# Performance work log

Measured on AMD Instinct MI355X. Metric: run time of the kernel, lower is better.

Reference implementation:

```python
import jax, jax.numpy as jnp
import numpy as np

B, S, D = 2, 2048, 1024
NH, NKV = 16, 4
HD = D // NH          # 64
NREP = NH // NKV      # 4
E, TOPK = 8, 2
CAP_FACTOR = 1.25
HID = 4 * D // 3      # 1365 (hardcoded in MoELayer)
EPS = 1e-6


def rmsnorm(x, w):
    xf = x.astype(jnp.float32)
    y = xf * jax.lax.rsqrt(jnp.mean(xf * xf, axis=-1, keepdims=True) + EPS)
    return y.astype(x.dtype) * w


def apply_rope(x, cos, sin):
    # x: [b, s, h, hd]; cos/sin: [1, s, 1, hd]
    half = x.shape[-1] // 2
    x1, x2 = x[..., :half], x[..., half:]
    ch, sh = cos[..., :half], sin[..., :half]
    return jnp.concatenate([x1 * ch - x2 * sh, x1 * sh + x2 * ch], axis=-1)


def swiglu(x, w1, w2, w3):
    return (jax.nn.silu(x @ w1) * (x @ w3)) @ w2


def setup_inputs():
    key = jax.random.key(0)
    ks = jax.random.split(key, 14)
    x = jax.random.normal(ks[0], (B, S, D), jnp.float32)
    # RoPE tables (standard 10000 base), duplicated halves so cos[..., :half] is valid
    pos = jnp.arange(S, dtype=jnp.float32)[:, None]
    inv = 1.0 / (10000.0 ** (jnp.arange(0, HD, 2, dtype=jnp.float32) / HD))  # [HD/2]
    ang = pos * inv[None, :]                                                # [S, HD/2]
    cos = jnp.concatenate([jnp.cos(ang), jnp.cos(ang)], -1)[None, :, None, :]
    sin = jnp.concatenate([jnp.sin(ang), jnp.sin(ang)], -1)[None, :, None, :]
    # causal additive mask [1,1,S,S]
    causal = jnp.tril(jnp.ones((S, S), bool))
    mask = jnp.where(causal, 0.0, -1e9).astype(jnp.float32)[None, None]
    s = 0.02
    return {
        'x': x, 'cos': cos, 'sin': sin, 'mask': mask,
        'attn_norm_w': jnp.ones((D,), jnp.float32),
        'moe_norm_w': jnp.ones((D,), jnp.float32),
        'wq': jax.random.normal(ks[1], (D, NH * HD), jnp.float32) * s,
        'wk': jax.random.normal(ks[2], (D, NKV * HD), jnp.float32) * s,
        'wv': jax.random.normal(ks[3], (D, NKV * HD), jnp.float32) * s,
        'wo': jax.random.normal(ks[4], (NH * HD, D), jnp.float32) * s,
        'router_w': jax.random.normal(ks[5], (D, E), jnp.float32) * s,
        'ew1': jax.random.normal(ks[6], (E, D, HID), jnp.float32) * s,
        'ew2': jax.random.normal(ks[7], (E, HID, D), jnp.float32) * s,
        'ew3': jax.random.normal(ks[8], (E, D, HID), jnp.float32) * s,
        'sw1': jax.random.normal(ks[9], (D, HID), jnp.float32) * s,
        'sw2': jax.random.normal(ks[10], (HID, D), jnp.float32) * s,
        'sw3': jax.random.normal(ks[11], (D, HID), jnp.float32) * s,
    }


def reference(x, cos, sin, mask, attn_norm_w, moe_norm_w, wq, wk, wv, wo,
              router_w, ew1, ew2, ew3, sw1, sw2, sw3):
    # ---- attention path ----
    xn = rmsnorm(x, attn_norm_w)
    q = (xn @ wq).reshape(B, S, NH, HD)
    k = (xn @ wk).reshape(B, S, NKV, HD)
    v = (xn @ wv).reshape(B, S, NKV, HD)
    q = apply_rope(q, cos, sin)
    k = apply_rope(k, cos, sin)
    new_k, new_v = k, v  # kv cache outputs (no prior cache)
    # repeat_interleave kv heads to NH
    k_rep = jnp.repeat(k, NREP, axis=2)  # [b,s,NH,hd]
    v_rep = jnp.repeat(v, NREP, axis=2)
    scores = jnp.einsum('bqhd,bkhd->bhqk', q, k_rep) / np.sqrt(HD)
    scores = scores + mask[:, :, -S:, :]
    attn = jax.nn.softmax(scores.astype(jnp.float32), axis=-1).astype(q.dtype)
    ao = jnp.einsum('bhqk,bkhd->bqhd', attn, v_rep).reshape(B, S, NH * HD)
    h = x + ao @ wo

    # ---- MoE path ----
    hn = rmsnorm(h, moe_norm_w)
    x_flat = hn.reshape(-1, D)            # [T, D]
    T = x_flat.shape[0]
    logits = x_flat @ router_w            # [T, E]
    probs = jax.nn.softmax(logits, axis=-1)
    w_topk, idx = jax.lax.top_k(probs, TOPK)          # [T, K]
    w_topk = w_topk / jnp.sum(w_topk, axis=-1, keepdims=True)
    onehot = jax.nn.one_hot(idx, E, dtype=jnp.float32)  # [T, K, E]
    counts = jnp.sum(onehot, axis=(0, 1))               # [E]
    util = jnp.mean((counts > 0).astype(jnp.float32)) * 100.0
    fraction = counts / T
    aux_loss = E * jnp.sum(jnp.mean(probs, axis=0) * fraction)
    capacity = int(T * TOPK / E * CAP_FACTOR)
    member = jnp.sum(onehot, axis=1) > 0                 # [T, E] token assigned to expert
    keep = member & (jnp.cumsum(member.astype(jnp.int32), axis=0) <= capacity)
    gate = jnp.sum(w_topk[:, :, None] * onehot, axis=1)  # [T, E] combine weights
    gate = gate * keep.astype(gate.dtype)
    # dense per-expert SwiGLU (same math as masked dispatch; zero-gated tokens vanish)
    h1 = jnp.einsum('td,edh->eth', x_flat, ew1)
    h3 = jnp.einsum('td,edh->eth', x_flat, ew3)
    eo = jnp.einsum('eth,ehd->etd', jax.nn.silu(h1) * h3, ew2)
    moe_out = jnp.einsum('etd,te->td', eo, gate).reshape(B, S, D)
    moe_out = moe_out + swiglu(hn, sw1, sw2, sw3)  # shared expert

    out = h + moe_out
    return out, aux_loss, util, new_k, new_v
```

## Files before the change

kernel.cpp:

```cpp
#include <hip/hip_runtime.h>
#include <hip/hip_bf16.h>
#include <math.h>

typedef __hip_bfloat16 bf16;
typedef __attribute__((ext_vector_type(8))) short short8;
typedef __attribute__((ext_vector_type(4))) float floatx4;

#define SEQ    2048
#define TTOK   4096
#define DM     1024
#define NHEAD  16
#define NKVH   4
#define HD     64
#define NEXP   8
#define HIDDEN 1365
#define HIDP   1408
#define CAPT   1280
#define NSLOT  (NEXP*CAPT)
#define TSLOT  (NSLOT+TTOK)
#define XPE    (CAPT/128)
#define XBT    14

__device__ __forceinline__ void gld16(const void* g, void* l) {
  __builtin_amdgcn_global_load_lds((const __attribute__((address_space(1))) void*)g,
                                   (__attribute__((address_space(3))) void*)l,
                                   16, 0, 0);
}

struct __align__(8) bf4 { bf16 x, y, z, w; };

struct EpiAux {
  const float* cosb; const float* sinb;
  bf16* qb; bf16* kb; bf16* vb; float* newk; float* newv;
};

__global__ __launch_bounds__(256) void transpose_cvt(
    const float* __restrict__ src, bf16* __restrict__ dst,
    int K, int N, int Kp, long srcZ, long dstZ) {
  src += (size_t)blockIdx.z * srcZ;
  dst += (size_t)blockIdx.z * dstZ;
  __shared__ float tile[64][65];
  const int tid = threadIdx.x;
  const int k0 = blockIdx.y * 64, n0 = blockIdx.x * 64;
  const int lr = tid >> 4, lc = (tid & 15) * 4;
#pragma unroll
  for (int i = 0; i < 4; ++i) {
    int k = k0 + lr + i * 16;
    int n = n0 + lc;
    float4 v = {0.f, 0.f, 0.f, 0.f};
    if (k < K) {
      if (n + 3 < N) v = *(const float4*)(src + (size_t)k * N + n);
      else {
        float* vp = (float*)&v;
        for (int e = 0; e < 4; ++e) if (n + e < N) vp[e] = src[(size_t)k * N + n + e];
      }
    }
    tile[lr + i * 16][lc] = v.x; tile[lr + i * 16][lc + 1] = v.y;
    tile[lr + i * 16][lc + 2] = v.z; tile[lr + i * 16][lc + 3] = v.w;
  }
  __syncthreads();
  const int n = tid >> 2, kk0 = (tid & 3) * 16;
  if (n0 + n < N) {
    bf16 buf[16];
#pragma unroll
    for (int e = 0; e < 16; ++e) buf[e] = (bf16)tile[kk0 + e][n];
    bf16* dp = dst + (size_t)(n0 + n) * Kp + k0 + kk0;
    *(short8*)dp = *(short8*)buf;
    *(short8*)(dp + 8) = *(short8*)(buf + 8);
  }
}

__global__ __launch_bounds__(256) void rmsnorm_kernel(
    const float* __restrict__ x, const float* __restrict__ w, bf16* __restrict__ out) {
  int t = blockIdx.x;
  const float* xr = x + (size_t)t * DM;
  float4 xv = *(const float4*)(xr + threadIdx.x * 4);
  float ss = xv.x * xv.x + xv.y * xv.y + xv.z * xv.z + xv.w * xv.w;
#pragma unroll
  for (int off = 1; off < 64; off <<= 1) ss += __shfl_xor(ss, off);
  __shared__ float sred[4];
  if ((threadIdx.x & 63) == 0) sred[threadIdx.x >> 6] = ss;
  __syncthreads();
  float scale = rsqrtf((sred[0] + sred[1] + sred[2] + sred[3]) * (1.f / DM) + 1e-6f);
  float4 wv = *(const float4*)(w + threadIdx.x * 4);
  bf4 o;
  o.x = (bf16)(xv.x * scale * wv.x); o.y = (bf16)(xv.y * scale * wv.y);
  o.z = (bf16)(xv.z * scale * wv.z); o.w = (bf16)(xv.w * scale * wv.w);
  ((bf4*)(out + (size_t)t * DM))[threadIdx.x] = o;
}

__global__ __launch_bounds__(256) void rmsnorm_router_kernel(
    const float* __restrict__ x, const float* __restrict__ w, const float* __restrict__ rw,
    bf16* __restrict__ out, float* __restrict__ probs,
    int* __restrict__ tIdx, float* __restrict__ tW) {
  int t = blockIdx.x;
  int tid = threadIdx.x, lane = tid & 63, wv = tid >> 6;
  const float* xr = x + (size_t)t * DM;
  float4 xv = *(const float4*)(xr + tid * 4);
  float ss = xv.x * xv.x + xv.y * xv.y + xv.z * xv.z + xv.w * xv.w;
#pragma unroll
  for (int off = 1; off < 64; off <<= 1) ss += __shfl_xor(ss, off);
  __shared__ float sred[4];
  __shared__ float red[4][8];
  if (lane == 0) sred[wv] = ss;
  __syncthreads();
  float scale = rsqrtf((sred[0] + sred[1] + sred[2] + sred[3]) * (1.f / DM) + 1e-6f);
  float4 wvv = *(const float4*)(w + tid * 4);
  float y[4] = {xv.x * scale * wvv.x, xv.y * scale * wvv.y,
                xv.z * scale * wvv.z, xv.w * scale * wvv.w};
  bf4 o; o.x = (bf16)y[0]; o.y = (bf16)y[1]; o.z = (bf16)y[2]; o.w = (bf16)y[3];
  ((bf4*)(out + (size_t)t * DM))[tid] = o;
  float acc[8] = {0, 0, 0, 0, 0, 0, 0, 0};
#pragma unroll
  for (int dd = 0; dd < 4; ++dd) {
    const float* rwr = rw + (size_t)(tid * 4 + dd) * 8;
#pragma unroll
    for (int e = 0; e < 8; ++e) acc[e] += y[dd] * rwr[e];
  }
#pragma unroll
  for (int e = 0; e < 8; ++e)
#pragma unroll
    for (int off = 1; off < 64; off <<= 1) acc[e] += __shfl_xor(acc[e], off);
  if (lane == 0)
#pragma unroll
    for (int e = 0; e < 8; ++e) red[wv][e] = acc[e];
  __syncthreads();
  if (tid == 0) {
    float lg[8];
#pragma unroll
    for (int e = 0; e < 8; ++e) lg[e] = red[0][e] + red[1][e] + red[2][e] + red[3][e];
    float mx = lg[0];
#pragma unroll
    for (int e = 1; e < 8; ++e) mx = fmaxf(mx, lg[e]);
    float p[8], se = 0.f;
#pragma unroll
    for (int e = 0; e < 8; ++e) { p[e] = __expf(lg[e] - mx); se += p[e]; }
#pragma unroll
    for (int e = 0; e < 8; ++e) { p[e] /= se; probs[t * 8 + e] = p[e]; }
    int i1 = 0;
#pragma unroll
    for (int e = 1; e < 8; ++e) if (p[e] > p[i1]) i1 = e;
    int i2 = (i1 == 0) ? 1 : 0;
#pragma unroll
    for (int e = 0; e < 8; ++e) if (e != i1 && p[e] > p[i2]) i2 = e;
    float s = p[i1] + p[i2];
    tIdx[t * 2] = i1; tIdx[t * 2 + 1] = i2;
    tW[t * 2] = p[i1] / s; tW[t * 2 + 1] = p[i2] / s;
  }
}

template <int EPI>
__global__ __launch_bounds__(256) void gemm_bt(
    const bf16* __restrict__ A, const bf16* __restrict__ Bt,
    int M, int N, int K, int lda, int ldb, int xPerXcd,
    float* __restrict__ Cf, int ldc,
    const float* __restrict__ resid, EpiAux aux) {
  __shared__ __align__(16) bf16 As[128 * 64];
  __shared__ __align__(16) bf16 Bs[128 * 64];
  const int tid = threadIdx.x, lane = tid & 63, wave = tid >> 6;
  const int f = blockIdx.x, lo = f >> 3;
  int xb = (f & 7) * xPerXcd + lo % xPerXcd;
  int n0 = (lo / xPerXcd) * 128;
  int m0 = xb * 128;

  const bf16* aSrc[4]; const bf16* bSrc[4];
  bf16* aDst[4]; bf16* bDst[4];
#pragma unroll
  for (int it = 0; it < 4; ++it) {
    int c = it * 256 + tid;
    int r = c >> 3, q = c & 7;
    int kq = q ^ (r & 7);
    aSrc[it] = A + (long)(m0 + r) * lda + kq * 8;
    bSrc[it] = Bt + (long)(n0 + r) * ldb + kq * 8;
    aDst[it] = As + (size_t)(it * 256 + wave * 64) * 8;
    bDst[it] = Bs + (size_t)(it * 256 + wave * 64) * 8;
  }

  floatx4 acc[4][4];
#pragma unroll
  for (int i = 0; i < 4; ++i)
#pragma unroll
    for (int j = 0; j < 4; ++j) { floatx4 z = {0.f, 0.f, 0.f, 0.f}; acc[i][j] = z; }

  const int wm = (wave & 1) * 64, wn = (wave >> 1) * 64;
  const int l15 = lane & 15, quad = lane >> 4;
  int aOff[4][2], bOff[4][2];
#pragma unroll
  for (int i = 0; i < 4; ++i) {
    int m = wm + i * 16 + l15;
    int n = wn + i * 16 + l15;
#pragma unroll
    for (int h = 0; h < 2; ++h) {
      aOff[i][h] = (((m << 3) | ((h * 4 + quad) ^ (m & 7))) << 3);
      bOff[i][h] = (((n << 3) | ((h * 4 + quad) ^ (n & 7))) << 3);
    }
  }

  const int kIters = K >> 6;
  for (int kt = 0; kt < kIters; ++kt) {
    __syncthreads();
#pragma unroll
    for (int it = 0; it < 4; ++it) {
      gld16(aSrc[it], aDst[it]);
      gld16(bSrc[it], bDst[it]);
      aSrc[it] += 64; bSrc[it] += 64;
    }
    __syncthreads();
#pragma unroll
    for (int h = 0; h < 2; ++h) {
      short8 af[4], bfr[4];
#pragma unroll
      for (int i = 0; i < 4; ++i) af[i] = *(const short8*)(As + aOff[i][h]);
#pragma unroll
      for (int j = 0; j < 4; ++j) bfr[j] = *(const short8*)(Bs + bOff[j][h]);
#pragma unroll
      for (int i = 0; i < 4; ++i)
#pragma unroll
        for (int j = 0; j < 4; ++j)
          acc[i][j] = __builtin_amdgcn_mfma_f32_16x16x32_bf16(af[i], bfr[j], acc[i][j], 0, 0, 0);
    }
  }

  if constexpr (EPI == 4) {
#pragma unroll
    for (int i = 0; i < 4; ++i) {
#pragma unroll
      for (int r = 0; r < 4; ++r) {
        int row = wm + i * 16 + quad * 4 + r;
        int t = m0 + row;
        int s = t & (SEQ - 1);
        if (n0 < 1024) {
#pragma unroll
          for (int j = 0; j < 2; ++j) {
            int col = n0 + wn + j * 16 + l15;
            int dlo = col & 63;
            float x1 = acc[i][j][r], x2 = acc[i][j + 2][r];
            float ch = aux.cosb[s * 64 + dlo], sh = aux.sinb[s * 64 + dlo];
            aux.qb[(size_t)t * DM + col]      = (bf16)((x1 * ch - x2 * sh) * 0.125f);
            aux.qb[(size_t)t * DM + col + 32] = (bf16)((x1 * sh + x2 * ch) * 0.125f);
          }
        } else if (n0 < 1280) {
#pragma unroll
          for (int j = 0; j < 2; ++j) {
            int ck = n0 + wn + j * 16 + l15 - 1024;
            int dlo = ck & 63;
            float x1 = acc[i][j][r], x2 = acc[i][j + 2][r];
            float ch = aux.cosb[s * 64 + dlo], sh = aux.sinb[s * 64 + dlo];
            float o1 = x1 * ch - x2 * sh, o2 = x1 * sh + x2 * ch;
            aux.kb[(size_t)t * 256 + ck]        = (bf16)o1;
            aux.kb[(size_t)t * 256 + ck + 32]   = (bf16)o2;
            aux.newk[(size_t)t * 256 + ck]      = o1;
            aux.newk[(size_t)t * 256 + ck + 32] = o2;
          }
        } else {
#pragma unroll
          for (int j = 0; j < 4; ++j) {
            int cv = n0 + wn + j * 16 + l15 - 1280;
            float v = acc[i][j][r];
            aux.vb[(size_t)t * 256 + cv]   = (bf16)v;
            aux.newv[(size_t)t * 256 + cv] = v;
          }
        }
      }
    }
    return;
  }
#pragma unroll
  for (int i = 0; i < 4; ++i) {
#pragma unroll
    for (int j = 0; j < 4; ++j) {
      int col = n0 + wn + j * 16 + l15;
#pragma unroll
      for (int r = 0; r < 4; ++r) {
        int row = wm + i * 16 + quad * 4 + r;
        size_t o = (size_t)(m0 + row) * ldc + col;
        Cf[o] = resid[o] + acc[i][j][r];
      }
    }
  }
}

__device__ __forceinline__ bool slot_block(
    int f, int NY, const int* neCnt, int& expert, int& m0, int& mLimit, int& n0) {
  int xcd = f & 7, lo = f >> 3;
  int xb = lo / NY, y = lo % NY;
  n0 = y * 64;
  if (xb < XPE) {
    expert = xcd;
    int ne = neCnt[xcd];
    if (xb * 128 >= ne) return false;
    m0 = xcd * CAPT + xb * 128;
    mLimit = ne - xb * 128;
    if (mLimit > 128) mLimit = 128;
  } else {
    expert = 8;
    int sb = xcd * 4 + (xb - XPE);
    m0 = NSLOT + sb * 128;
    mLimit = 128;
  }
  return true;
}

__global__ __launch_bounds__(256) void gemm_dual9(
    const bf16* __restrict__ A, const bf16* __restrict__ B1t, const bf16* __restrict__ B3t,
    bf16* __restrict__ mact,
    const int* __restrict__ tokList, const int* __restrict__ neCnt) {
  __shared__ __align__(16) bf16 As[128 * 64];
  __shared__ __align__(16) bf16 B1s[64 * 64];
  __shared__ __align__(16) bf16 B3s[64 * 64];
  const int tid = threadIdx.x, lane = tid & 63, wave = tid >> 6;
  int expert, m0, mLimit, n0;
  if (!slot_block(blockIdx.x, 22, neCnt, expert, m0, mLimit, n0)) return;
  const bf16* B1e = B1t + (long)expert * (HIDDEN * 1024);
  const bf16* B3e = B3t + (long)expert * (HIDDEN * 1024);

  const bf16* aSrc[4]; const bf16* b1Src[2]; const bf16* b3Src[2];
  bf16* aDst[4]; bf16* b1Dst[2]; bf16* b3Dst[2];
#pragma unroll
  for (int it = 0; it < 4; ++it) {
    int c = it * 256 + tid;
    int r = c >> 3, q = c & 7;
    int kq = q ^ (r & 7);
    int rr = r < mLimit ? r : (mLimit - 1);
    aSrc[it] = A + (long)tokList[m0 + rr] * 1024 + kq * 8;
    aDst[it] = As + (size_t)(it * 256 + wave * 64) * 8;
  }
#pragma unroll
  for (int it = 0; it < 2; ++it) {
    int c = it * 256 + tid;
    int r = c >> 3, q = c & 7;
    int kq = q ^ (r & 7);
    int nn = n0 + r; if (nn > HIDDEN - 1) nn = HIDDEN - 1;
    b1Src[it] = B1e + (long)nn * 1024 + kq * 8;
    b3Src[it] = B3e + (long)nn * 1024 + kq * 8;
    b1Dst[it] = B1s + (size_t)(it * 256 + wave * 64) * 8;
    b3Dst[it] = B3s + (size_t)(it * 256 + wave * 64) * 8;
  }

  floatx4 acc1[4][2], acc3[4][2];
#pragma unroll
  for (int i = 0; i < 4; ++i)
#pragma unroll
    for (int j = 0; j < 2; ++j) {
      floatx4 z = {0.f, 0.f, 0.f, 0.f};
      acc1[i][j] = z; acc3[i][j] = z;
    }

  const int wm = (wave & 1) * 64, wn = (wave >> 1) * 32;
  const int l15 = lane & 15, quad = lane >> 4;
  int aOff[4][2], bOff[2][2];
#pragma unroll
  for (int h = 0; h < 2; ++h) {
#pragma unroll
    for (int i = 0; i < 4; ++i) {
      int m = wm + i * 16 + l15;
      aOff[i][h] = (((m << 3) | ((h * 4 + quad) ^ (m & 7))) << 3);
    }
#pragma unroll
    for (int j = 0; j < 2; ++j) {
      int n = wn + j * 16 + l15;
      bOff[j][h] = (((n << 3) | ((h * 4 + quad) ^ (n & 7))) << 3);
    }
  }

  for (int kt = 0; kt < 16; ++kt) {
    __syncthreads();
#pragma unroll
    for (int it = 0; it < 4; ++it) { gld16(aSrc[it], aDst[it]); aSrc[it] += 64; }
#pragma unroll
    for (int it = 0; it < 2; ++it) {
      gld16(b1Src[it], b1Dst[it]); b1Src[it] += 64;
      gld16(b3Src[it], b3Dst[it]); b3Src[it] += 64;
    }
    __syncthreads();
#pragma unroll
    for (int h = 0; h < 2; ++h) {
      short8 af[4];
#pragma unroll
      for (int i = 0; i < 4; ++i) af[i] = *(const short8*)(As + aOff[i][h]);
#pragma unroll
      for (int j = 0; j < 2; ++j) {
        short8 b1f = *(const short8*)(B1s + bOff[j][h]);
        short8 b3f = *(const short8*)(B3s + bOff[j][h]);
#pragma unroll
        for (int i = 0; i < 4; ++i) {
          acc1[i][j] = __builtin_amdgcn_mfma_f32_16x16x32_bf16(af[i], b1f, acc1[i][j], 0, 0, 0);
          acc3[i][j] = __builtin_amdgcn_mfma_f32_16x16x32_bf16(af[i], b3f, acc3[i][j], 0, 0, 0);
        }
      }
    }
  }

#pragma unroll
  for (int i = 0; i < 4; ++i) {
#pragma unroll
    for (int j = 0; j < 2; ++j) {
      int col = n0 + wn + j * 16 + l15;
#pragma unroll
      for (int r = 0; r < 4; ++r) {
        int row = wm + i * 16 + quad * 4 + r;
        if (row >= mLimit) continue;
        float a1 = acc1[i][j][r], a3 = acc3[i][j][r];
        float sl = a1 / (1.f + __expf(-a1));
        mact[(size_t)(m0 + row) * HIDP + col] = (col < HIDDEN) ? (bf16)(sl * a3) : (bf16)0.f;
      }
    }
  }
}

__global__ __launch_bounds__(256) void gemm_down9(
    const bf16* __restrict__ A, const bf16* __restrict__ B2t,
    bf16* __restrict__ eo,
    const float* __restrict__ gateW, const int* __restrict__ neCnt) {
  __shared__ __align__(16) bf16 As[128 * 64];
  __shared__ __align__(16) bf16 Bs[64 * 64];
  const int tid = threadIdx.x, lane = tid & 63, wave = tid >> 6;
  int expert, m0, mLimit, n0;
  if (!slot_block(blockIdx.x, 16, neCnt, expert, m0, mLimit, n0)) return;
  const bf16* Be = B2t + (long)expert * (1024 * HIDP);

  const bf16* aSrc[4]; const bf16* bSrc[2];
  bf16* aDst[4]; bf16* bDst[2];
#pragma unroll
  for (int it = 0; it < 4; ++it) {
    int c = it * 256 + tid;
    int r = c >> 3, q = c & 7;
    int kq = q ^ (r & 7);
    int rr = r < mLimit ? r : (mLimit - 1);
    aSrc[it] = A + (long)(m0 + rr) * HIDP + kq * 8;
    aDst[it] = As + (size_t)(it * 256 + wave * 64) * 8;
  }
#pragma unroll
  for (int it = 0; it < 2; ++it) {
    int c = it * 256 + tid;
    int r = c >> 3, q = c & 7;
    int kq = q ^ (r & 7);
    bSrc[it] = Be + (long)(n0 + r) * HIDP + kq * 8;
    bDst[it] = Bs + (size_t)(it * 256 + wave * 64) * 8;
  }

  floatx4 acc[4][2];
#pragma unroll
  for (int i = 0; i < 4; ++i)
#pragma unroll
    for (int j = 0; j < 2; ++j) { floatx4 z = {0.f, 0.f, 0.f, 0.f}; acc[i][j] = z; }

  const int wm = (wave & 1) * 64, wn = (wave >> 1) * 32;
  const int l15 = lane & 15, quad = lane >> 4;
  int aOff[4][2], bOff[2][2];
#pragma unroll
  for (int h = 0; h < 2; ++h) {
#pragma unroll
    for (int i = 0; i < 4; ++i) {
      int m = wm + i * 16 + l15;
      aOff[i][h] = (((m << 3) | ((h * 4 + quad) ^ (m & 7))) << 3);
    }
#pragma unroll
    for (int j = 0; j < 2; ++j) {
      int n = wn + j * 16 + l15;
      bOff[j][h] = (((n << 3) | ((h * 4 + quad) ^ (n & 7))) << 3);
    }
  }

  for (int kt = 0; kt < 22; ++kt) {
    __syncthreads();
#pragma unroll
    for (int it = 0; it < 4; ++it) { gld16(aSrc[it], aDst[it]); aSrc[it] += 64; }
#pragma unroll
    for (int it = 0; it < 2; ++it) { gld16(bSrc[it], bDst[it]); bSrc[it] += 64; }
    __syncthreads();
#pragma unroll
    for (int h = 0; h < 2; ++h) {
      short8 af[4];
#pragma unroll
      for (int i = 0; i < 4; ++i) af[i] = *(const short8*)(As + aOff[i][h]);
#pragma unroll
      for (int j = 0; j < 2; ++j) {
        short8 bf = *(const short8*)(Bs + bOff[j][h]);
#pragma unroll
        for (int i = 0; i < 4; ++i)
          acc[i][j] = __builtin_amdgcn_mfma_f32_16x16x32_bf16(af[i], bf, acc[i][j], 0, 0, 0);
      }
    }
  }

#pragma unroll
  for (int i = 0; i < 4; ++i) {
#pragma unroll
    for (int j = 0; j < 2; ++j) {
      int col = n0 + wn + j * 16 + l15;
#pragma unroll
      for (int r = 0; r < 4; ++r) {
        int row = wm + i * 16 + quad * 4 + r;
        if (row >= mLimit) continue;
        eo[(size_t)(m0 + row) * 1024 + col] = (bf16)(gateW[m0 + row] * acc[i][j][r]);
      }
    }
  }
}

__global__ __launch_bounds__(256) void vt_kernel(
    const bf16* __restrict__ vb, bf16* __restrict__ vt) {
  __shared__ __align__(16) bf16 tile[64 * 72];
  int t0 = blockIdx.x * 64, bg = blockIdx.y;
  int b = bg >> 2, g = bg & 3;
  int tid = threadIdx.x;
  for (int c = tid; c < 512; c += 256) {
    int r = c >> 3, d8 = (c & 7) * 8;
    *(short8*)(tile + r * 72 + d8) =
        *(const short8*)(vb + (size_t)(b * SEQ + t0 + r) * 256 + g * 64 + d8);
  }
  __syncthreads();
  for (int c = tid; c < 512; c += 256) {
    int d = c >> 3, s8 = (c & 7) * 8;
    bf16 tmp[8];
#pragma unroll
    for (int x = 0; x < 8; ++x) tmp[x] = tile[(s8 + x) * 72 + d];
    *(short8*)(vt + ((size_t)bg * 64 + d) * SEQ + t0 + s8) = *(short8*)tmp;
  }
}

__global__ __launch_bounds__(256) void attn_kernel(
    const bf16* __restrict__ Q, const bf16* __restrict__ Kc, const bf16* __restrict__ Vt,
    bf16* __restrict__ AO) {
  __shared__ __align__(16) bf16 Qs[64 * 64];
  __shared__ __align__(16) bf16 Ks[64 * 64];
  __shared__ __align__(16) bf16 Vs[64 * 64];
  __shared__ __align__(16) bf16 Ps[4][16 * 64];
  const int pairI = blockIdx.x, h = blockIdx.y, b = blockIdx.z;
  const int g = h >> 2;
  const int tid = threadIdx.x, lane = tid & 63, wave = tid >> 6;
  const int l15 = lane & 15, quad = lane >> 4;

  const bf16* kSrc[2]; const bf16* vSrc[2]; bf16* kDst[2]; bf16* vDst[2];
#pragma unroll
  for (int it = 0; it < 2; ++it) {
    int c = it * 256 + tid;
    int r = c >> 3, p = c & 7;
    int kq = p ^ (r & 7);
    kSrc[it] = Kc + (size_t)(b * SEQ + r) * 256 + g * 64 + kq * 8;
    vSrc[it] = Vt + ((size_t)(b * 4 + g) * 64 + r) * SEQ + kq * 8;
    kDst[it] = Ks + (size_t)(it * 256 + wave * 64) * 8;
    vDst[it] = Vs + (size_t)(it * 256 + wave * 64) * 8;
  }

  int qOff[2], kvOff[4][2], pOff[2];
#pragma unroll
  for (int hh = 0; hh < 2; ++hh) {
    int m = wave * 16 + l15;
    qOff[hh] = (m << 6) + (((hh * 4 + quad) ^ (m & 7)) << 3);
#pragma unroll
    for (int j = 0; j < 4; ++j) {
      int n = j * 16 + l15;
      kvOff[j][hh] = (n << 6) + (((hh * 4 + quad) ^ (n & 7)) << 3);
    }
    int cblk = (hh * 2 + (quad >> 1)) ^ (l15 >> 2);
    pOff[hh] = (l15 << 6) + (cblk << 4) + ((quad & 1) << 3);
  }
  bf16* pw = &Ps[wave][0];
  const int rowl = wave * 16 + quad * 4;

  short8 onesb;
#pragma unroll
  for (int e = 0; e < 8; ++e) onesb[e] = (short)0x3F80;

  for (int ph = 0; ph < 2; ++ph) {
    const int q0 = (ph == 0 ? pairI : 31 - pairI) * 64;
    __syncthreads();
#pragma unroll
    for (int it = 0; it < 2; ++it) {
      int c = it * 256 + tid;
      int r = c >> 3, p = c & 7;
      int kq = p ^ (r & 7);
      gld16(Q + (size_t)(b * SEQ + q0 + r) * DM + h * 64 + kq * 8,
            Qs + (size_t)(it * 256 + wave * 64) * 8);
    }

    floatx4 oacc[4], sumacc;
#pragma unroll
    for (int r = 0; r < 4; ++r) { floatx4 z = {0.f, 0.f, 0.f, 0.f}; oacc[r] = z; }
    { floatx4 z = {0.f, 0.f, 0.f, 0.f}; sumacc = z; }

    const int nkt = (q0 >> 6) + 1;
    for (int kt = 0; kt < nkt; ++kt) {
      __syncthreads();
#pragma unroll
      for (int it = 0; it < 2; ++it) {
        gld16(kSrc[it] + (size_t)kt * 64 * 256, kDst[it]);
        gld16(vSrc[it] + kt * 64, vDst[it]);
      }
      __syncthreads();

      floatx4 sacc[4];
#pragma unroll
      for (int j = 0; j < 4; ++j) { floatx4 z = {0.f, 0.f, 0.f, 0.f}; sacc[j] = z; }
#pragma unroll
      for (int hh = 0; hh < 2; ++hh) {
        short8 aq = *(const short8*)(Qs + qOff[hh]);
#pragma unroll
        for (int j = 0; j < 4; ++j)
          sacc[j] = __builtin_amdgcn_mfma_f32_16x16x32_bf16(
              aq, *(const short8*)(Ks + kvOff[j][hh]), sacc[j], 0, 0, 0);
      }

      const bool lastTile = (kt == nkt - 1);
#pragma unroll
      for (int j = 0; j < 4; ++j) {
        int sw = ((j ^ quad) << 4) + l15;
        int colg = j * 16 + l15;
#pragma unroll
        for (int r = 0; r < 4; ++r) {
          float p = __expf(sacc[j][r]);
          if (lastTile && colg > rowl + r) p = 0.f;
          pw[(quad * 4 + r) * 64 + sw] = (bf16)p;
        }
      }
      asm volatile("s_waitcnt lgkmcnt(0)" ::: "memory");
#pragma unroll
      for (int hh = 0; hh < 2; ++hh) {
        short8 ap = *(const short8*)(pw + pOff[hh]);
#pragma unroll
        for (int j = 0; j < 4; ++j)
          oacc[j] = __builtin_amdgcn_mfma_f32_16x16x32_bf16(
              ap, *(const short8*)(Vs + kvOff[j][hh]), oacc[j], 0, 0, 0);
        sumacc = __builtin_amdgcn_mfma_f32_16x16x32_bf16(ap, onesb, sumacc, 0, 0, 0);
      }
    }

    float inv[4];
#pragma unroll
    for (int r = 0; r < 4; ++r) inv[r] = 1.f / sumacc[r];
#pragma unroll
    for (int j = 0; j < 4; ++j)
#pragma unroll
      for (int r = 0; r < 4; ++r) {
        int t = b * SEQ + q0 + rowl + r;
        AO[(size_t)t * DM + h * 64 + j * 16 + l15] = (bf16)(oacc[j][r] * inv[r]);
      }
  }
}

__global__ __launch_bounds__(256) void assign_kernel(
    const int* __restrict__ tIdx, const float* __restrict__ tW,
    int* __restrict__ tokList, float* __restrict__ gateW,
    int* __restrict__ neCnt, int* __restrict__ cntFull, int* __restrict__ slotOf) {
  int e = blockIdx.x;
  int tid = threadIdx.x, lane = tid & 63, wv = tid >> 6;
  if (e == 8) {
    for (int t = tid; t < TTOK; t += 256) {
      tokList[NSLOT + t] = t;
      gateW[NSLOT + t] = 1.0f;
    }
    if (tid == 0) neCnt[8] = TTOK;
    return;
  }
  __shared__ int waveTot[4];
  __shared__ int offs;
  if (tid == 0) offs = 0;
  __syncthreads();
  for (int base = 0; base < TTOK; base += 256) {
    int t = base + tid;
    int a = tIdx[t * 2], b2 = tIdx[t * 2 + 1];
    bool sel = (a == e) || (b2 == e);
    unsigned long long mask = __ballot(sel);
    int wrank = __popcll(mask & ((1ull << lane) - 1ull));
    if (lane == 0) waveTot[wv] = __popcll(mask);
    __syncthreads();
    int pre = offs;
    for (int w2 = 0; w2 < wv; ++w2) pre += waveTot[w2];
    int rank = pre + wrank;
    if (sel && rank < CAPT) {
      int slot = e * CAPT + rank;
      tokList[slot] = t;
      gateW[slot] = (a == e) ? tW[t * 2] : tW[t * 2 + 1];
      slotOf[t * 2 + ((a == e) ? 0 : 1)] = slot;
    }
    __syncthreads();
    if (tid == 0) offs += waveTot[0] + waveTot[1] + waveTot[2] + waveTot[3];
    __syncthreads();
  }
  if (tid == 0) {
    cntFull[e] = offs;
    neCnt[e] = offs < CAPT ? offs : CAPT;
  }
}

__global__ __launch_bounds__(256) void aux_kernel(
    const float* __restrict__ probs, const int* __restrict__ cntFull,
    float* __restrict__ outAux) {
  __shared__ float psum[8];
  if (threadIdx.x < 8) psum[threadIdx.x] = 0.f;
  __syncthreads();
  float lp[8] = {0, 0, 0, 0, 0, 0, 0, 0};
  for (int t = threadIdx.x; t < TTOK; t += 256) {
#pragma unroll
    for (int e = 0; e < 8; ++e) lp[e] += probs[t * 8 + e];
  }
#pragma unroll
  for (int e = 0; e < 8; ++e)
#pragma unroll
    for (int off = 1; off < 64; off <<= 1) lp[e] += __shfl_xor(lp[e], off);
  if ((threadIdx.x & 63) == 0)
#pragma unroll
    for (int e = 0; e < 8; ++e) atomicAdd(&psum[e], lp[e]);
  __syncthreads();
  if (threadIdx.x == 0) {
    float aux = 0.f; int used = 0;
    for (int e = 0; e < 8; ++e) {
      aux += (psum[e] / (float)TTOK) * ((float)cntFull[e] / (float)TTOK);
      if (cntFull[e] > 0) used++;
    }
    outAux[0] = 8.f * aux;
    outAux[1] = 100.f * (float)used / 8.f;
  }
}

__global__ __launch_bounds__(256) void combine_kernel(
    float* __restrict__ outp, const float* __restrict__ hbuf,
    const bf16* __restrict__ eo, const int* __restrict__ slotOf) {
  int t = blockIdx.x, tid = threadIdx.x;
  float4 v = ((const float4*)(hbuf + (size_t)t * DM))[tid];
  bf4 sh = ((const bf4*)(eo + (size_t)(NSLOT + t) * DM))[tid];
  v.x += (float)sh.x; v.y += (float)sh.y; v.z += (float)sh.z; v.w += (float)sh.w;
  int s0 = slotOf[t * 2], s1 = slotOf[t * 2 + 1];
  if (s0 >= 0) {
    bf4 e = ((const bf4*)(eo + (size_t)s0 * DM))[tid];
    v.x += (float)e.x; v.y += (float)e.y; v.z += (float)e.z; v.w += (float)e.w;
  }
  if (s1 >= 0) {
    bf4 e = ((const bf4*)(eo + (size_t)s1 * DM))[tid];
    v.x += (float)e.x; v.y += (float)e.y; v.z += (float)e.z; v.w += (float)e.w;
  }
  ((float4*)(outp + (size_t)t * DM))[tid] = v;
}

extern "C" void kernel_launch(void* const* d_in, const int* in_sizes, int n_in,
                              void* d_out, int out_size, void* d_ws, size_t ws_size,
                              hipStream_t stream) {
  (void)in_sizes; (void)n_in; (void)out_size; (void)ws_size;
  const float* x     = (const float*)d_in[0];
  const float* cosb  = (const float*)d_in[1];
  const float* sinb  = (const float*)d_in[2];
  const float* attnw = (const float*)d_in[4];
  const float* moew  = (const float*)d_in[5];
  const float* wq  = (const float*)d_in[6];
  const float* wk  = (const float*)d_in[7];
  const float* wv  = (const float*)d_in[8];
  const float* wo  = (const float*)d_in[9];
  const float* rw  = (const float*)d_in[10];
  const float* ew1 = (const float*)d_in[11];
  const float* ew2 = (const float*)d_in[12];
  const float* ew3 = (const float*)d_in[13];
  const float* sw1 = (const float*)d_in[14];
  const float* sw2 = (const float*)d_in[15];
  const float* sw3 = (const float*)d_in[16];

  float* outp = (float*)d_out;
  float* auxp = outp + 4194304;
  float* newk = outp + 4194306;
  float* newv = newk + 1048576;

  char* wsp = (char*)d_ws;
  size_t off = 0;
  auto alloc = [&](size_t bytes) -> void* {
    void* p = wsp + off; off += (bytes + 255) & ~(size_t)255; return p;
  };
  bf16* wqkvT = (bf16*)alloc((size_t)1536 * 1024 * 2);
  bf16* woT   = (bf16*)alloc((size_t)1024 * 1024 * 2);
  bf16* ew1T  = (bf16*)alloc((size_t)9 * HIDDEN * 1024 * 2);
  bf16* ew3T  = (bf16*)alloc((size_t)9 * HIDDEN * 1024 * 2);
  bf16* ew2T  = (bf16*)alloc((size_t)9 * 1024 * HIDP * 2);
  bf16* xn    = (bf16*)alloc((size_t)TTOK * DM * 2);
  bf16* qb    = (bf16*)alloc((size_t)TTOK * DM * 2);
  bf16* kb    = (bf16*)alloc((size_t)TTOK * 256 * 2);
  bf16* vb    = (bf16*)alloc((size_t)TTOK * 256 * 2);
  bf16* vt    = (bf16*)alloc((size_t)TTOK * 256 * 2);
  bf16* ao    = (bf16*)alloc((size_t)TTOK * DM * 2);
  float* hbuf = (float*)alloc((size_t)TTOK * DM * 4);
  bf16* hn    = (bf16*)alloc((size_t)TTOK * DM * 2);
  float* probs = (float*)alloc((size_t)TTOK * 8 * 4);
  int*   tIdx  = (int*)alloc((size_t)TTOK * 2 * 4);
  float* tW    = (float*)alloc((size_t)TTOK * 2 * 4);
  int*   tokList = (int*)alloc((size_t)TSLOT * 4);
  float* gateW   = (float*)alloc((size_t)TSLOT * 4);
  int*   neCnt   = (int*)alloc(64);
  int*   cntFull = (int*)alloc(64);
  int*   slotOf  = (int*)alloc((size_t)TTOK * 2 * 4);
  bf16*  mact = (bf16*)alloc((size_t)TSLOT * HIDP * 2);
  bf16*  eo   = (bf16*)alloc((size_t)TSLOT * DM * 2);

  EpiAux nil{};
  EpiAux ropeAux{cosb, sinb, qb, kb, vb, newk, newv};

  transpose_cvt<<<dim3(16, 16, 1), 256, 0, stream>>>(wq, wqkvT, 1024, 1024, 1024, 0, 0);
  transpose_cvt<<<dim3(4, 16, 1), 256, 0, stream>>>(wk, wqkvT + (size_t)1024 * 1024, 1024, 256, 1024, 0, 0);
  transpose_cvt<<<dim3(4, 16, 1), 256, 0, stream>>>(wv, wqkvT + (size_t)1280 * 1024, 1024, 256, 1024, 0, 0);
  transpose_cvt<<<dim3(16, 16, 1), 256, 0, stream>>>(wo, woT, 1024, 1024, 1024, 0, 0);
  transpose_cvt<<<dim3(22, 16, NEXP), 256, 0, stream>>>(ew1, ew1T, 1024, HIDDEN, 1024,
      (long)1024 * HIDDEN, (long)HIDDEN * 1024);
  transpose_cvt<<<dim3(22, 16, NEXP), 256, 0, stream>>>(ew3, ew3T, 1024, HIDDEN, 1024,
      (long)1024 * HIDDEN, (long)HIDDEN * 1024);
  transpose_cvt<<<dim3(16, 22, NEXP), 256, 0, stream>>>(ew2, ew2T, HIDDEN, 1024, HIDP,
      (long)HIDDEN * 1024, (long)1024 * HIDP);
  transpose_cvt<<<dim3(22, 16, 1), 256, 0, stream>>>(sw1, ew1T + (size_t)8 * HIDDEN * 1024,
      1024, HIDDEN, 1024, 0, 0);
  transpose_cvt<<<dim3(22, 16, 1), 256, 0, stream>>>(sw3, ew3T + (size_t)8 * HIDDEN * 1024,
      1024, HIDDEN, 1024, 0, 0);
  transpose_cvt<<<dim3(16, 22, 1), 256, 0, stream>>>(sw2, ew2T + (size_t)8 * 1024 * HIDP,
      HIDDEN, 1024, HIDP, 0, 0);

  rmsnorm_kernel<<<TTOK, 256, 0, stream>>>(x, attnw, xn);
  gemm_bt<4><<<8 * 4 * 12, 256, 0, stream>>>(
      xn, wqkvT, TTOK, 1536, 1024, 1024, 1024, 4, nullptr, 0, nullptr, ropeAux);
  vt_kernel<<<dim3(32, 8), 256, 0, stream>>>(vb, vt);
  attn_kernel<<<dim3(16, NHEAD, 2), 256, 0, stream>>>(qb, kb, vt, ao);
  gemm_bt<2><<<8 * 4 * 8, 256, 0, stream>>>(
      ao, woT, TTOK, 1024, 1024, 1024, 1024, 4, hbuf, 1024, x, nil);

  rmsnorm_router_kernel<<<TTOK, 256, 0, stream>>>(hbuf, moew, rw, hn, probs, tIdx, tW);
  hipMemsetAsync(slotOf, 0xFF, (size_t)TTOK * 2 * 4, stream);
  assign_kernel<<<9, 256, 0, stream>>>(tIdx, tW, tokList, gateW, neCnt, cntFull, slotOf);
  aux_kernel<<<1, 256, 0, stream>>>(probs, cntFull, auxp);

  gemm_dual9<<<8 * XBT * 22, 256, 0, stream>>>(hn, ew1T, ew3T, mact, tokList, neCnt);
  gemm_down9<<<8 * XBT * 16, 256, 0, stream>>>(mact, ew2T, eo, gateW, neCnt);
  combine_kernel<<<TTOK, 256, 0, stream>>>(outp, hbuf, eo, slotOf);
}
```

Before: 583.2 us.

## Widen MoE gate/up GEMM tile, double-buffer attention KV, enlarge transpose tiles

The fused gate/up expert GEMM now computes 128x128 output tiles instead of 128x64, halving the block count and reusing each A tile across twice as many columns, with launch bounds raised to two blocks per CU. The attention kernel double-buffers its K/V shared tiles, prefetching the next tile while computing the current one. The weight transpose-convert kernel processes 128-row K tiles per block to cut block count. These changes trade higher register and LDS pressure, and fewer blocks for load balance, for less redundant global traffic and better latency hiding.

```diff
diff --git a/kernel.cpp b/kernel.cpp
--- a/kernel.cpp
+++ b/kernel.cpp
@@ -39,12 +39,12 @@
     int K, int N, int Kp, long srcZ, long dstZ) {
   src += (size_t)blockIdx.z * srcZ;
   dst += (size_t)blockIdx.z * dstZ;
-  __shared__ float tile[64][65];
+  __shared__ float tile[128][65];
   const int tid = threadIdx.x;
-  const int k0 = blockIdx.y * 64, n0 = blockIdx.x * 64;
+  const int k0 = blockIdx.y * 128, n0 = blockIdx.x * 64;
   const int lr = tid >> 4, lc = (tid & 15) * 4;
 #pragma unroll
-  for (int i = 0; i < 4; ++i) {
+  for (int i = 0; i < 8; ++i) {
     int k = k0 + lr + i * 16;
     int n = n0 + lc;
     float4 v = {0.f, 0.f, 0.f, 0.f};
@@ -59,14 +59,14 @@
     tile[lr + i * 16][lc + 2] = v.z; tile[lr + i * 16][lc + 3] = v.w;
   }
   __syncthreads();
-  const int n = tid >> 2, kk0 = (tid & 3) * 16;
+  const int n = tid >> 2, kk0 = (tid & 3) * 32;
   if (n0 + n < N) {
-    bf16 buf[16];
-#pragma unroll
-    for (int e = 0; e < 16; ++e) buf[e] = (bf16)tile[kk0 + e][n];
+    bf16 buf[32];
+#pragma unroll
+    for (int e = 0; e < 32; ++e) buf[e] = (bf16)tile[kk0 + e][n];
     bf16* dp = dst + (size_t)(n0 + n) * Kp + k0 + kk0;
-    *(short8*)dp = *(short8*)buf;
-    *(short8*)(dp + 8) = *(short8*)(buf + 8);
+#pragma unroll
+    for (int c = 0; c < 4; ++c) *(short8*)(dp + c * 8) = *(short8*)(buf + c * 8);
   }
 }
 
@@ -301,21 +301,22 @@
   return true;
 }
 
-__global__ __launch_bounds__(256) void gemm_dual9(
+__global__ __launch_bounds__(256, 2) void gemm_dual9(
     const bf16* __restrict__ A, const bf16* __restrict__ B1t, const bf16* __restrict__ B3t,
     bf16* __restrict__ mact,
     const int* __restrict__ tokList, const int* __restrict__ neCnt) {
   __shared__ __align__(16) bf16 As[128 * 64];
-  __shared__ __align__(16) bf16 B1s[64 * 64];
-  __shared__ __align__(16) bf16 B3s[64 * 64];
+  __shared__ __align__(16) bf16 B1s[128 * 64];
+  __shared__ __align__(16) bf16 B3s[128 * 64];
   const int tid = threadIdx.x, lane = tid & 63, wave = tid >> 6;
   int expert, m0, mLimit, n0;
-  if (!slot_block(blockIdx.x, 22, neCnt, expert, m0, mLimit, n0)) return;
+  if (!slot_block(blockIdx.x, 11, neCnt, expert, m0, mLimit, n0)) return;
+  n0 <<= 1;
   const bf16* B1e = B1t + (long)expert * (HIDDEN * 1024);
   const bf16* B3e = B3t + (long)expert * (HIDDEN * 1024);
 
-  const bf16* aSrc[4]; const bf16* b1Src[2]; const bf16* b3Src[2];
-  bf16* aDst[4]; bf16* b1Dst[2]; bf16* b3Dst[2];
+  const bf16* aSrc[4]; const bf16* b1Src[4]; const bf16* b3Src[4];
+  bf16* aDst[4]; bf16* b1Dst[4]; bf16* b3Dst[4];
 #pragma unroll
   for (int it = 0; it < 4; ++it) {
     int c = it * 256 + tid;
@@ -324,12 +325,6 @@
     int rr = r < mLimit ? r : (mLimit - 1);
     aSrc[it] = A + (long)tokList[m0 + rr] * 1024 + kq * 8;
     aDst[it] = As + (size_t)(it * 256 + wave * 64) * 8;
-  }
-#pragma unroll
-  for (int it = 0; it < 2; ++it) {
-    int c = it * 256 + tid;
-    int r = c >> 3, q = c & 7;
-    int kq = q ^ (r & 7);
     int nn = n0 + r; if (nn > HIDDEN - 1) nn = HIDDEN - 1;
     b1Src[it] = B1e + (long)nn * 1024 + kq * 8;
     b3Src[it] = B3e + (long)nn * 1024 + kq * 8;
@@ -337,18 +332,18 @@
     b3Dst[it] = B3s + (size_t)(it * 256 + wave * 64) * 8;
   }
 
-  floatx4 acc1[4][2], acc3[4][2];
+  floatx4 acc1[4][4], acc3[4][4];
 #pragma unroll
   for (int i = 0; i < 4; ++i)
 #pragma unroll
-    for (int j = 0; j < 2; ++j) {
+    for (int j = 0; j < 4; ++j) {
       floatx4 z = {0.f, 0.f, 0.f, 0.f};
       acc1[i][j] = z; acc3[i][j] = z;
     }
 
-  const int wm = (wave & 1) * 64, wn = (wave >> 1) * 32;
+  const int wm = (wave & 1) * 64, wn = (wave >> 1) * 64;
   const int l15 = lane & 15, quad = lane >> 4;
-  int aOff[4][2], bOff[2][2];
+  int aOff[4][2], bOff[4][2];
 #pragma unroll
   for (int h = 0; h < 2; ++h) {
 #pragma unroll
@@ -357,7 +352,7 @@
       aOff[i][h] = (((m << 3) | ((h * 4 + quad) ^ (m & 7))) << 3);
     }
 #pragma unroll
-    for (int j = 0; j < 2; ++j) {
+    for (int j = 0; j < 4; ++j) {
       int n = wn + j * 16 + l15;
       bOff[j][h] = (((n << 3) | ((h * 4 + quad) ^ (n & 7))) << 3);
     }
@@ -368,7 +363,7 @@
 #pragma unroll
     for (int it = 0; it < 4; ++it) { gld16(aSrc[it], aDst[it]); aSrc[it] += 64; }
 #pragma unroll
-    for (int it = 0; it < 2; ++it) {
+    for (int it = 0; it < 4; ++it) {
       gld16(b1Src[it], b1Dst[it]); b1Src[it] += 64;
       gld16(b3Src[it], b3Dst[it]); b3Src[it] += 64;
     }
@@ -379,7 +374,7 @@
 #pragma unroll
       for (int i = 0; i < 4; ++i) af[i] = *(const short8*)(As + aOff[i][h]);
 #pragma unroll
-      for (int j = 0; j < 2; ++j) {
+      for (int j = 0; j < 4; ++j) {
         short8 b1f = *(const short8*)(B1s + bOff[j][h]);
         short8 b3f = *(const short8*)(B3s + bOff[j][h]);
 #pragma unroll
@@ -394,7 +389,7 @@
 #pragma unroll
   for (int i = 0; i < 4; ++i) {
 #pragma unroll
-    for (int j = 0; j < 2; ++j) {
+    for (int j = 0; j < 4; ++j) {
       int col = n0 + wn + j * 16 + l15;
 #pragma unroll
       for (int r = 0; r < 4; ++r) {
@@ -524,8 +519,8 @@
     const bf16* __restrict__ Q, const bf16* __restrict__ Kc, const bf16* __restrict__ Vt,
     bf16* __restrict__ AO) {
   __shared__ __align__(16) bf16 Qs[64 * 64];
-  __shared__ __align__(16) bf16 Ks[64 * 64];
-  __shared__ __align__(16) bf16 Vs[64 * 64];
+  __shared__ __align__(16) bf16 Ks[2][64 * 64];
+  __shared__ __align__(16) bf16 Vs[2][64 * 64];
   __shared__ __align__(16) bf16 Ps[4][16 * 64];
   const int pairI = blockIdx.x, h = blockIdx.y, b = blockIdx.z;
   const int g = h >> 2;
@@ -540,8 +535,8 @@
     int kq = p ^ (r & 7);
     kSrc[it] = Kc + (size_t)(b * SEQ + r) * 256 + g * 64 + kq * 8;
     vSrc[it] = Vt + ((size_t)(b * 4 + g) * 64 + r) * SEQ + kq * 8;
-    kDst[it] = Ks + (size_t)(it * 256 + wave * 64) * 8;
-    vDst[it] = Vs + (size_t)(it * 256 + wave * 64) * 8;
+    kDst[it] = &Ks[0][0] + (size_t)(it * 256 + wave * 64) * 8;
+    vDst[it] = &Vs[0][0] + (size_t)(it * 256 + wave * 64) * 8;
   }
 
   int qOff[2], kvOff[4][2], pOff[2];
@@ -575,6 +570,11 @@
       gld16(Q + (size_t)(b * SEQ + q0 + r) * DM + h * 64 + kq * 8,
             Qs + (size_t)(it * 256 + wave * 64) * 8);
     }
+#pragma unroll
+    for (int it = 0; it < 2; ++it) {
+      gld16(kSrc[it], kDst[it]);
+      gld16(vSrc[it], vDst[it]);
+    }
 
     floatx4 oacc[4], sumacc;
 #pragma unroll
@@ -583,11 +583,18 @@
 
     const int nkt = (q0 >> 6) + 1;
     for (int kt = 0; kt < nkt; ++kt) {
-      __syncthreads();
-#pragma unroll
-      for (int it = 0; it < 2; ++it) {
-        gld16(kSrc[it] + (size_t)kt * 64 * 256, kDst[it]);
-        gld16(vSrc[it] + kt * 64, vDst[it]);
+      const int cb = kt & 1;
+      const int bufOff = cb * 4096;
+      if (kt + 1 < nkt) {
+        const int nb = (cb ^ 1) * 4096;
+#pragma unroll
+        for (int it = 0; it < 2; ++it) {
+          gld16(kSrc[it] + (size_t)(kt + 1) * 64 * 256, kDst[it] + nb);
+          gld16(vSrc[it] + (kt + 1) * 64, vDst[it] + nb);
+        }
+        asm volatile("s_waitcnt vmcnt(4)" ::: "memory");
+      } else {
+        asm volatile("s_waitcnt vmcnt(0)" ::: "memory");
       }
       __syncthreads();
 
@@ -600,7 +607,7 @@
 #pragma unroll
         for (int j = 0; j < 4; ++j)
           sacc[j] = __builtin_amdgcn_mfma_f32_16x16x32_bf16(
-              aq, *(const short8*)(Ks + kvOff[j][hh]), sacc[j], 0, 0, 0);
+              aq, *(const short8*)(&Ks[0][0] + bufOff + kvOff[j][hh]), sacc[j], 0, 0, 0);
       }
 
       const bool lastTile = (kt == nkt - 1);
@@ -622,9 +629,10 @@
 #pragma unroll
         for (int j = 0; j < 4; ++j)
           oacc[j] = __builtin_amdgcn_mfma_f32_16x16x32_bf16(
-              ap, *(const short8*)(Vs + kvOff[j][hh]), oacc[j], 0, 0, 0);
+              ap, *(const short8*)(&Vs[0][0] + bufOff + kvOff[j][hh]), oacc[j], 0, 0, 0);
         sumacc = __builtin_amdgcn_mfma_f32_16x16x32_bf16(ap, onesb, sumacc, 0, 0, 0);
       }
+      __syncthreads();
     }
 
     float inv[4];
@@ -792,21 +800,21 @@
   EpiAux nil{};
   EpiAux ropeAux{cosb, sinb, qb, kb, vb, newk, newv};
 
-  transpose_cvt<<<dim3(16, 16, 1), 256, 0, stream>>>(wq, wqkvT, 1024, 1024, 1024, 0, 0);
-  transpose_cvt<<<dim3(4, 16, 1), 256, 0, stream>>>(wk, wqkvT + (size_t)1024 * 1024, 1024, 256, 1024, 0, 0);
-  transpose_cvt<<<dim3(4, 16, 1), 256, 0, stream>>>(wv, wqkvT + (size_t)1280 * 1024, 1024, 256, 1024, 0, 0);
-  transpose_cvt<<<dim3(16, 16, 1), 256, 0, stream>>>(wo, woT, 1024, 1024, 1024, 0, 0);
-  transpose_cvt<<<dim3(22, 16, NEXP), 256, 0, stream>>>(ew1, ew1T, 1024, HIDDEN, 1024,
+  transpose_cvt<<<dim3(16, 8, 1), 256, 0, stream>>>(wq, wqkvT, 1024, 1024, 1024, 0, 0);
+  transpose_cvt<<<dim3(4, 8, 1), 256, 0, stream>>>(wk, wqkvT + (size_t)1024 * 1024, 1024, 256, 1024, 0, 0);
+  transpose_cvt<<<dim3(4, 8, 1), 256, 0, stream>>>(wv, wqkvT + (size_t)1280 * 1024, 1024, 256, 1024, 0, 0);
+  transpose_cvt<<<dim3(16, 8, 1), 256, 0, stream>>>(wo, woT, 1024, 1024, 1024, 0, 0);
+  transpose_cvt<<<dim3(22, 8, NEXP), 256, 0, stream>>>(ew1, ew1T, 1024, HIDDEN, 1024,
       (long)1024 * HIDDEN, (long)HIDDEN * 1024);
-  transpose_cvt<<<dim3(22, 16, NEXP), 256, 0, stream>>>(ew3, ew3T, 1024, HIDDEN, 1024,
+  transpose_cvt<<<dim3(22, 8, NEXP), 256, 0, stream>>>(ew3, ew3T, 1024, HIDDEN, 1024,
       (long)1024 * HIDDEN, (long)HIDDEN * 1024);
-  transpose_cvt<<<dim3(16, 22, NEXP), 256, 0, stream>>>(ew2, ew2T, HIDDEN, 1024, HIDP,
+  transpose_cvt<<<dim3(16, 11, NEXP), 256, 0, stream>>>(ew2, ew2T, HIDDEN, 1024, HIDP,
       (long)HIDDEN * 1024, (long)1024 * HIDP);
-  transpose_cvt<<<dim3(22, 16, 1), 256, 0, stream>>>(sw1, ew1T + (size_t)8 * HIDDEN * 1024,
+  transpose_cvt<<<dim3(22, 8, 1), 256, 0, stream>>>(sw1, ew1T + (size_t)8 * HIDDEN * 1024,
       1024, HIDDEN, 1024, 0, 0);
-  transpose_cvt<<<dim3(22, 16, 1), 256, 0, stream>>>(sw3, ew3T + (size_t)8 * HIDDEN * 1024,
+  transpose_cvt<<<dim3(22, 8, 1), 256, 0, stream>>>(sw3, ew3T + (size_t)8 * HIDDEN * 1024,
       1024, HIDDEN, 1024, 0, 0);
-  transpose_cvt<<<dim3(16, 22, 1), 256, 0, stream>>>(sw2, ew2T + (size_t)8 * 1024 * HIDP,
+  transpose_cvt<<<dim3(16, 11, 1), 256, 0, stream>>>(sw2, ew2T + (size_t)8 * 1024 * HIDP,
       HIDDEN, 1024, HIDP, 0, 0);
 
   rmsnorm_kernel<<<TTOK, 256, 0, stream>>>(x, attnw, xn);
@@ -822,7 +830,7 @@
   assign_kernel<<<9, 256, 0, stream>>>(tIdx, tW, tokList, gateW, neCnt, cntFull, slotOf);
   aux_kernel<<<1, 256, 0, stream>>>(probs, cntFull, auxp);
 
-  gemm_dual9<<<8 * XBT * 22, 256, 0, stream>>>(hn, ew1T, ew3T, mact, tokList, neCnt);
+  gemm_dual9<<<8 * XBT * 11, 256, 0, stream>>>(hn, ew1T, ew3T, mact, tokList, neCnt);
   gemm_down9<<<8 * XBT * 16, 256, 0, stream>>>(mact, ew2T, eo, gateW, neCnt);
   combine_kernel<<<TTOK, 256, 0, stream>>>(outp, hbuf, eo, slotOf);
 }
```

Result: slower. 607.9 us (+4.2%).
